# Kernel optimization log

Hardware: AMD Instinct MI355X
Metric: run time of the kernel (lower is better)

Reference implementation:

```python
import jax, jax.numpy as jnp
import numpy as np
from jax import lax

E_NUM, R_NUM = 100000, 500
ENT_DIM = 200
OUT_CH = 16
EPS = 1e-5


def _bn(x, s, b, m, v, axis):
    # eval-mode batchnorm; params broadcast along `axis`
    shape = [1] * x.ndim
    shape[axis] = x.shape[axis]
    s, b, m, v = (p.reshape(shape) for p in (s, b, m, v))
    return (x - m) * (s * lax.rsqrt(v + EPS)) + b


def setup_inputs() -> dict:
    key = jax.random.key(0)
    ks = jax.random.split(key, 12)
    B = 1024
    inp = {
        'entity_id': jax.random.randint(ks[0], (B,), 0, E_NUM),
        'relation_id': jax.random.randint(ks[1], (B,), 0, R_NUM),
        'ent_emb': jax.random.normal(ks[2], (E_NUM, ENT_DIM), jnp.float32) * 0.02,
        'rel_emb': jax.random.normal(ks[3], (R_NUM, ENT_DIM), jnp.float32) * 0.02,
        'filt_w': jax.random.normal(ks[4], (R_NUM, OUT_CH * 9), jnp.float32) * 0.1,
        'filt1_w': jax.random.normal(ks[5], (R_NUM, OUT_CH * 9), jnp.float32) * 0.1,
        'fc_w': jax.random.normal(ks[6], (ENT_DIM, 20 * 20 * OUT_CH * 2), jnp.float32) * 0.01,
        'fc_b': jnp.zeros((ENT_DIM,), jnp.float32),
        'out_bias': jnp.zeros((E_NUM,), jnp.float32),
    }
    for name, c, i in (('bn0', 1, 7), ('bn1', OUT_CH, 8), ('bn2', ENT_DIM, 9)):
        k1, k2, k3 = jax.random.split(ks[i], 3)
        inp[name + '_s'] = 1.0 + 0.1 * jax.random.normal(k1, (c,), jnp.float32)
        inp[name + '_b'] = 0.1 * jax.random.normal(k2, (c,), jnp.float32)
        inp[name + '_m'] = 0.1 * jax.random.normal(k3, (c,), jnp.float32)
        inp[name + '_v'] = jnp.ones((c,), jnp.float32)
    return inp


def reference(entity_id, relation_id, ent_emb, rel_emb, filt_w, filt1_w, fc_w, fc_b,
              out_bias, bn0_s, bn0_b, bn0_m, bn0_v, bn1_s, bn1_b, bn1_m, bn1_v,
              bn2_s, bn2_b, bn2_m, bn2_v):
    B = entity_id.shape[0]
    e = ent_emb[entity_id]                         # [B, 200]
    r = rel_emb[relation_id]                       # [B, 200]
    f = filt_w[relation_id].reshape(B * OUT_CH, 1, 3, 3)
    f1 = filt1_w[relation_id].reshape(B * OUT_CH, 1, 1, 9)

    x = jnp.concatenate([e, r], 1).reshape(B, 1, 10, 40)
    c0, c1, c2, c3 = jnp.split(x, 4, axis=3)       # each [B,1,10,10]
    t1 = jnp.swapaxes(c1, 2, 3)
    t2 = jnp.swapaxes(c3, 2, 3)
    m = jnp.concatenate([c0, c2], 2)               # [B,1,20,10]
    n = jnp.concatenate([t2, t1], 2)               # [B,1,20,10]
    x = jnp.concatenate([m, n], 3)                 # [B,1,20,20]

    x = _bn(x, bn0_s, bn0_b, bn0_m, bn0_v, axis=1)
    x = jnp.transpose(x, (1, 0, 2, 3))             # [1,B,20,20]

    dn = ('NCHW', 'OIHW', 'NCHW')
    x1 = lax.conv_general_dilated(x, f, (1, 1), [(1, 1), (1, 1)],
                                  dimension_numbers=dn, feature_group_count=B)
    x1 = _bn(x1.reshape(B, OUT_CH, 20, 20), bn1_s, bn1_b, bn1_m, bn1_v, axis=1)
    x2 = lax.conv_general_dilated(x, f1, (1, 1), [(0, 0), (4, 4)],
                                  dimension_numbers=dn, feature_group_count=B)
    x2 = _bn(x2.reshape(B, OUT_CH, 20, 20), bn1_s, bn1_b, bn1_m, bn1_v, axis=1)

    x = jax.nn.relu(jnp.concatenate([x1, x2], axis=1)).reshape(B, -1)  # [B,12800]
    x = x @ fc_w.T + fc_b                          # [B,200]
    x = _bn(x, bn2_s, bn2_b, bn2_m, bn2_v, axis=1)
    x = jax.nn.relu(x)
    logits = x @ ent_emb.T + out_bias              # [B, E_NUM]
    return jax.nn.sigmoid(logits)
```

## Files before the change

### kernel.cpp

```cpp
#include <hip/hip_runtime.h>
#include <hip/hip_bf16.h>

#define EPS 1e-5f

typedef __bf16 bf16x8 __attribute__((ext_vector_type(8)));
typedef float f32x4 __attribute__((ext_vector_type(4)));
typedef unsigned short ushort_t;

#define GLDS16(gp, lp) __builtin_amdgcn_global_load_lds( \
    (const __attribute__((address_space(1))) unsigned int*)(gp), \
    (__attribute__((address_space(3))) unsigned int*)(lp), 16, 0, 0)

__device__ __forceinline__ unsigned short f2bf(float f) {
    unsigned int u = __float_as_uint(f);
    u += 0x7fffu + ((u >> 16) & 1u);
    return (unsigned short)(u >> 16);
}

__device__ __forceinline__ void convert_pad_body(
    const float* __restrict__ src, ushort_t* __restrict__ dst,
    int R, int C, int R2, int C2, long long start, long long stride)
{
    int cpr = C2 >> 2;
    long long nchunks = (long long)R2 * cpr;
    for (long long idx = start; idx < nchunks; idx += stride) {
        int row = (int)(idx / cpr);
        int col = ((int)(idx - (long long)row * cpr)) << 2;
        float4 v = make_float4(0.f, 0.f, 0.f, 0.f);
        if (row < R && col < C)
            v = *reinterpret_cast<const float4*>(src + (size_t)row * C + col);
        union { unsigned short h[4]; uint2 u; } pk;
        pk.h[0] = f2bf(v.x); pk.h[1] = f2bf(v.y);
        pk.h[2] = f2bf(v.z); pk.h[3] = f2bf(v.w);
        *reinterpret_cast<uint2*>(dst + (size_t)row * C2 + col) = pk.u;
    }
}

__global__ __launch_bounds__(256) void prep_all_kernel(
    const float* __restrict__ fc_w, ushort_t* __restrict__ fcw,
    const int* __restrict__ eid, const int* __restrict__ rid,
    const float* __restrict__ ent_emb, const float* __restrict__ rel_emb,
    const float* __restrict__ filt_w, const float* __restrict__ filt1_w,
    const float* __restrict__ bn0_s, const float* __restrict__ bn0_b,
    const float* __restrict__ bn0_m, const float* __restrict__ bn0_v,
    const float* __restrict__ bn1_s, const float* __restrict__ bn1_b,
    const float* __restrict__ bn1_m, const float* __restrict__ bn1_v,
    ushort_t* __restrict__ act, ushort_t* __restrict__ E_bf)
{
    __shared__ float img[20][20];
    __shared__ float fA[16][9];
    __shared__ float fB[16][9];
    __shared__ float a1[16], b1[16];

    int t = threadIdx.x;
    if (blockIdx.x >= 4224) {
        long long start = (long long)(blockIdx.x - 4224) * 256 + t;
        convert_pad_body(ent_emb, E_bf, 100000, 200, 100000, 224, start, 21875LL * 256);
        return;
    }
    if (blockIdx.x >= 1024) {
        long long start = (long long)(blockIdx.x - 1024) * 256 + t;
        convert_pad_body(fc_w, fcw, 200, 12800, 256, 12800, start, 3200LL * 256);
        return;
    }

    int b = blockIdx.x;
    int e = eid[b], r = rid[b];

    float a0 = bn0_s[0] * rsqrtf(bn0_v[0] + EPS);
    float c0 = bn0_b[0] - bn0_m[0] * a0;

    for (int p = t; p < 400; p += 256) {
        int i = p / 20, j = p - (p / 20) * 20;
        int src;
        if (i < 10) src = (j < 10) ? (i * 40 + j) : ((j - 10) * 40 + 30 + i);
        else        src = (j < 10) ? ((i - 10) * 40 + 20 + j) : ((j - 10) * 40 + 10 + (i - 10));
        float v = (src < 200) ? ent_emb[(size_t)e * 200 + src]
                              : rel_emb[(size_t)r * 200 + (src - 200)];
        img[i][j] = v * a0 + c0;
    }
    for (int p = t; p < 144; p += 256) fA[p / 9][p % 9] = filt_w[(size_t)r * 144 + p];
    for (int p = t; p < 144; p += 256) fB[p / 9][p % 9] = filt1_w[(size_t)r * 144 + p];
    if (t < 16) {
        float a = bn1_s[t] * rsqrtf(bn1_v[t] + EPS);
        a1[t] = a;
        b1[t] = bn1_b[t] - bn1_m[t] * a;
    }
    __syncthreads();

    for (int idx = t; idx < 12800; idx += 256) {
        int c = idx / 400;
        int p = idx - c * 400;
        int i = p / 20, j = p - (p / 20) * 20;
        int ch = c & 15;
        float acc = 0.f;
        if (c < 16) {
            #pragma unroll
            for (int di = 0; di < 3; ++di) {
                int ii = i + di - 1;
                if (ii < 0 || ii >= 20) continue;
                #pragma unroll
                for (int dj = 0; dj < 3; ++dj) {
                    int jj = j + dj - 1;
                    if (jj >= 0 && jj < 20) acc += img[ii][jj] * fA[ch][di * 3 + dj];
                }
            }
        } else {
            #pragma unroll
            for (int dj = 0; dj < 9; ++dj) {
                int jj = j + dj - 4;
                if (jj >= 0 && jj < 20) acc += img[i][jj] * fB[ch][dj];
            }
        }
        float v = fmaxf(acc * a1[ch] + b1[ch], 0.f);
        act[(size_t)b * 12800 + idx] = f2bf(v);
    }
}

__global__ __launch_bounds__(256) void fc_gemm_kernel(
    const ushort_t* __restrict__ act,
    const ushort_t* __restrict__ fcw,
    float* __restrict__ part)
{
    __shared__ ushort_t lA[128 * 64];
    __shared__ ushort_t lB[64 * 64];

    int t = threadIdx.x;
    int bx = blockIdx.x;
    int mt = bx & 7;
    int nt = (bx >> 3) & 3;
    int ks = bx >> 5;
    int m0 = mt * 128, n0 = nt * 64, k0 = ks * 640;

    int lane = t & 63, w = t >> 6;
    int wm = (w >> 1) * 64;
    int wn = (w & 1) * 32;

    f32x4 acc[4][2] = {};

    for (int step = 0; step < 10; ++step) {
        int kk = k0 + step * 64;
        for (int c = w; c < 16; c += 4) {
            int elem = c * 512 + lane * 8;
            int row = elem >> 6, col = elem & 63;
            GLDS16(act + (size_t)(m0 + row) * 12800 + kk + col, lA + c * 512);
        }
        for (int c = w; c < 8; c += 4) {
            int elem = c * 512 + lane * 8;
            int row = elem >> 6, col = elem & 63;
            GLDS16(fcw + (size_t)(n0 + row) * 12800 + kk + col, lB + c * 512);
        }
        __syncthreads();
        #pragma unroll
        for (int kq = 0; kq < 2; ++kq) {
            bf16x8 af[4], bfr[2];
            #pragma unroll
            for (int mf = 0; mf < 4; ++mf) {
                int row = wm + mf * 16 + (lane & 15);
                af[mf] = *reinterpret_cast<const bf16x8*>(lA + row * 64 + kq * 32 + (lane >> 4) * 8);
            }
            #pragma unroll
            for (int nf = 0; nf < 2; ++nf) {
                int row = wn + nf * 16 + (lane & 15);
                bfr[nf] = *reinterpret_cast<const bf16x8*>(lB + row * 64 + kq * 32 + (lane >> 4) * 8);
            }
            #pragma unroll
            for (int mf = 0; mf < 4; ++mf)
                #pragma unroll
                for (int nf = 0; nf < 2; ++nf)
                    acc[mf][nf] = __builtin_amdgcn_mfma_f32_16x16x32_bf16(af[mf], bfr[nf], acc[mf][nf], 0, 0, 0);
        }
        __syncthreads();
    }

    float* outp = part + (size_t)ks * 1024 * 256;
    #pragma unroll
    for (int mf = 0; mf < 4; ++mf) {
        #pragma unroll
        for (int nf = 0; nf < 2; ++nf) {
            int colg = n0 + wn + nf * 16 + (lane & 15);
            int rowb = (lane >> 4) * 4;
            #pragma unroll
            for (int j = 0; j < 4; ++j) {
                int rowg = m0 + wm + mf * 16 + rowb + j;
                outp[(size_t)rowg * 256 + colg] = acc[mf][nf][j];
            }
        }
    }
}

__global__ __launch_bounds__(256) void reduce_bn2_kernel(
    const float* __restrict__ part, const float* __restrict__ fc_b,
    const float* __restrict__ bn2_s, const float* __restrict__ bn2_b,
    const float* __restrict__ bn2_m, const float* __restrict__ bn2_v,
    ushort_t* __restrict__ h)
{
    int idx = blockIdx.x * 256 + threadIdx.x;
    if (idx >= 1024 * 224) return;
    int m = idx / 224, n = idx - m * 224;
    float v = 0.f;
    if (n < 200) {
        float s = 0.f;
        #pragma unroll 4
        for (int k = 0; k < 20; ++k) s += part[(size_t)k * 1024 * 256 + (size_t)m * 256 + n];
        s += fc_b[n];
        float a = bn2_s[n] * rsqrtf(bn2_v[n] + EPS);
        v = fmaxf((s - bn2_m[n]) * a + bn2_b[n], 0.f);
    }
    h[idx] = f2bf(v);
}

__global__ __launch_bounds__(256) void big_gemm_kernel(
    const ushort_t* __restrict__ hm,
    const ushort_t* __restrict__ em,
    const float* __restrict__ out_bias,
    float* __restrict__ out)
{
    __shared__ ushort_t lA[2][128 * 32];
    __shared__ ushort_t lB[2][128 * 32];

    int phys = blockIdx.x;
    int virt = (phys & 7) * 782 + (phys >> 3);
    int mt = virt & 7;
    int nt = virt >> 3;
    int m0 = mt * 128, n0 = nt * 128;

    int t = threadIdx.x;
    int lane = t & 63, w = t >> 6;
    int wm = (w >> 1) * 64;
    int wn = (w & 1) * 64;

    f32x4 acc[4][4] = {};

    for (int c = w; c < 8; c += 4) {
        int row = c * 16 + (lane >> 2);
        int scol = ((lane & 3) ^ ((row >> 1) & 3)) * 8;
        GLDS16(hm + (size_t)(m0 + row) * 224 + scol, lA[0] + c * 512);
        int rowB = n0 + row; if (rowB > 99999) rowB = 99999;
        GLDS16(em + (size_t)rowB * 224 + scol, lB[0] + c * 512);
    }
    __syncthreads();

    for (int step = 0; step < 7; ++step) {
        int cur = step & 1;
        if (step < 6) {
            int kk = (step + 1) * 32;
            int nxt = cur ^ 1;
            for (int c = w; c < 8; c += 4) {
                int row = c * 16 + (lane >> 2);
                int scol = ((lane & 3) ^ ((row >> 1) & 3)) * 8;
                GLDS16(hm + (size_t)(m0 + row) * 224 + kk + scol, lA[nxt] + c * 512);
                int rowB = n0 + row; if (rowB > 99999) rowB = 99999;
                GLDS16(em + (size_t)rowB * 224 + kk + scol, lB[nxt] + c * 512);
            }
        }
        const ushort_t* A = lA[cur];
        const ushort_t* B = lB[cur];
        bf16x8 af[4], bfr[4];
        #pragma unroll
        for (int mf = 0; mf < 4; ++mf) {
            int r = wm + mf * 16 + (lane & 15);
            int pc = ((lane >> 4) ^ ((r >> 1) & 3)) * 8;
            af[mf] = *reinterpret_cast<const bf16x8*>(A + r * 32 + pc);
        }
        #pragma unroll
        for (int nf = 0; nf < 4; ++nf) {
            int r = wn + nf * 16 + (lane & 15);
            int pc = ((lane >> 4) ^ ((r >> 1) & 3)) * 8;
            bfr[nf] = *reinterpret_cast<const bf16x8*>(B + r * 32 + pc);
        }
        #pragma unroll
        for (int mf = 0; mf < 4; ++mf)
            #pragma unroll
            for (int nf = 0; nf < 4; ++nf)
                acc[mf][nf] = __builtin_amdgcn_mfma_f32_16x16x32_bf16(bfr[nf], af[mf], acc[mf][nf], 0, 0, 0);
        __syncthreads();
    }

    int ncol_base = n0 + wn + (lane >> 4) * 4;
    f32x4 b4[4];
    #pragma unroll
    for (int nf = 0; nf < 4; ++nf) {
        int colg = ncol_base + nf * 16;
        b4[nf] = (colg < 100000) ? *reinterpret_cast<const f32x4*>(out_bias + colg)
                                 : f32x4{0.f, 0.f, 0.f, 0.f};
    }
    #pragma unroll
    for (int mf = 0; mf < 4; ++mf) {
        int rowg = m0 + wm + mf * 16 + (lane & 15);
        float* orow = out + (size_t)rowg * 100000;
        #pragma unroll
        for (int nf = 0; nf < 4; ++nf) {
            int colg = ncol_base + nf * 16;
            if (colg < 100000) {
                f32x4 x = acc[mf][nf];
                f32x4 s;
                #pragma unroll
                for (int q = 0; q < 4; ++q)
                    s[q] = __builtin_amdgcn_rcpf(1.f + __expf(-(x[q] + b4[nf][q])));
                __builtin_nontemporal_store(s, reinterpret_cast<f32x4*>(orow + colg));
            }
        }
    }
}

extern "C" void kernel_launch(void* const* d_in, const int* in_sizes, int n_in,
                              void* d_out, int out_size, void* d_ws, size_t ws_size,
                              hipStream_t stream)
{
    const int*   eid      = (const int*)d_in[0];
    const int*   rid      = (const int*)d_in[1];
    const float* ent_emb  = (const float*)d_in[2];
    const float* rel_emb  = (const float*)d_in[3];
    const float* filt_w   = (const float*)d_in[4];
    const float* filt1_w  = (const float*)d_in[5];
    const float* fc_w     = (const float*)d_in[6];
    const float* fc_b     = (const float*)d_in[7];
    const float* out_bias = (const float*)d_in[8];
    const float* bn0_s = (const float*)d_in[9];
    const float* bn0_b = (const float*)d_in[10];
    const float* bn0_m = (const float*)d_in[11];
    const float* bn0_v = (const float*)d_in[12];
    const float* bn1_s = (const float*)d_in[13];
    const float* bn1_b = (const float*)d_in[14];
    const float* bn1_m = (const float*)d_in[15];
    const float* bn1_v = (const float*)d_in[16];
    const float* bn2_s = (const float*)d_in[17];
    const float* bn2_b = (const float*)d_in[18];
    const float* bn2_m = (const float*)d_in[19];
    const float* bn2_v = (const float*)d_in[20];
    float* out = (float*)d_out;

    char* ws = (char*)d_ws;
    ushort_t* E_bf = (ushort_t*)(ws + 0);
    ushort_t* act  = (ushort_t*)(ws + 44800000);
    ushort_t* fcw  = (ushort_t*)(ws + 71014400);
    float*    part = (float*)(ws + 77568000);
    ushort_t* hmat = (ushort_t*)(ws + 98539520);

    hipLaunchKernelGGL(prep_all_kernel, dim3(1024 + 3200 + 21875), dim3(256), 0, stream,
                       fc_w, fcw,
                       eid, rid, ent_emb, rel_emb, filt_w, filt1_w,
                       bn0_s, bn0_b, bn0_m, bn0_v, bn1_s, bn1_b, bn1_m, bn1_v, act, E_bf);
    hipLaunchKernelGGL(fc_gemm_kernel, dim3(640), dim3(256), 0, stream,
                       act, fcw, part);
    hipLaunchKernelGGL(reduce_bn2_kernel, dim3((1024 * 224) / 256), dim3(256), 0, stream,
                       part, fc_b, bn2_s, bn2_b, bn2_m, bn2_v, hmat);
    hipLaunchKernelGGL(big_gemm_kernel, dim3(782 * 8), dim3(256), 0, stream,
                       hmat, E_bf, out_bias, out);
}
```

Baseline: 209.5 us.

## Make big GEMM persistent and prefetch next tile's first K-slice

The output GEMM now launches 1280 persistent blocks that loop over the 6256 tiles with a grid stride, instead of one block per tile. During the last K step of each tile, the block prefetches the first K-slice of its next tile into the other LDS buffer, so that load overlaps the current MMA and epilogue. This removes per-block launch and prologue latency, at the cost of a possible tail imbalance (6256/1280 is not an integer) and less scheduler freedom across CUs.

```diff
diff --git a/kernel.cpp b/kernel.cpp
--- a/kernel.cpp
+++ b/kernel.cpp
@@ -219,88 +219,110 @@
     __shared__ ushort_t lA[2][128 * 32];
     __shared__ ushort_t lB[2][128 * 32];
 
-    int phys = blockIdx.x;
-    int virt = (phys & 7) * 782 + (phys >> 3);
-    int mt = virt & 7;
-    int nt = virt >> 3;
-    int m0 = mt * 128, n0 = nt * 128;
-
     int t = threadIdx.x;
     int lane = t & 63, w = t >> 6;
     int wm = (w >> 1) * 64;
     int wn = (w & 1) * 64;
-
-    f32x4 acc[4][4] = {};
-
-    for (int c = w; c < 8; c += 4) {
-        int row = c * 16 + (lane >> 2);
-        int scol = ((lane & 3) ^ ((row >> 1) & 3)) * 8;
-        GLDS16(hm + (size_t)(m0 + row) * 224 + scol, lA[0] + c * 512);
-        int rowB = n0 + row; if (rowB > 99999) rowB = 99999;
-        GLDS16(em + (size_t)rowB * 224 + scol, lB[0] + c * 512);
+    int srow = (lane >> 2);
+    int scol = ((lane & 3) ^ ((srow >> 1) & 3)) * 8;
+
+    int p = blockIdx.x;
+    int phase = 0;
+
+    {
+        int virt = (p & 7) * 782 + (p >> 3);
+        int m0 = (virt & 7) * 128, n0 = (virt >> 3) * 128;
+        for (int c = w; c < 8; c += 4) {
+            int row = c * 16 + srow;
+            GLDS16(hm + (size_t)(m0 + row) * 224 + scol, lA[0] + c * 512);
+            int rowB = n0 + row; if (rowB > 99999) rowB = 99999;
+            GLDS16(em + (size_t)rowB * 224 + scol, lB[0] + c * 512);
+        }
     }
     __syncthreads();
 
-    for (int step = 0; step < 7; ++step) {
-        int cur = step & 1;
-        if (step < 6) {
-            int kk = (step + 1) * 32;
+    for (int idx = p; idx < 6256; idx += 1280) {
+        int virt = (idx & 7) * 782 + (idx >> 3);
+        int m0 = (virt & 7) * 128, n0 = (virt >> 3) * 128;
+        int nidx = idx + 1280;
+        bool has_next = nidx < 6256;
+        int nm0 = 0, nn0 = 0;
+        if (has_next) {
+            int nvirt = (nidx & 7) * 782 + (nidx >> 3);
+            nm0 = (nvirt & 7) * 128; nn0 = (nvirt >> 3) * 128;
+        }
+
+        f32x4 acc[4][4] = {};
+
+        for (int step = 0; step < 7; ++step) {
+            int cur = (phase + step) & 1;
             int nxt = cur ^ 1;
-            for (int c = w; c < 8; c += 4) {
-                int row = c * 16 + (lane >> 2);
-                int scol = ((lane & 3) ^ ((row >> 1) & 3)) * 8;
-                GLDS16(hm + (size_t)(m0 + row) * 224 + kk + scol, lA[nxt] + c * 512);
-                int rowB = n0 + row; if (rowB > 99999) rowB = 99999;
-                GLDS16(em + (size_t)rowB * 224 + kk + scol, lB[nxt] + c * 512);
-            }
-        }
-        const ushort_t* A = lA[cur];
-        const ushort_t* B = lB[cur];
-        bf16x8 af[4], bfr[4];
-        #pragma unroll
-        for (int mf = 0; mf < 4; ++mf) {
-            int r = wm + mf * 16 + (lane & 15);
-            int pc = ((lane >> 4) ^ ((r >> 1) & 3)) * 8;
-            af[mf] = *reinterpret_cast<const bf16x8*>(A + r * 32 + pc);
-        }
-        #pragma unroll
-        for (int nf = 0; nf < 4; ++nf) {
-            int r = wn + nf * 16 + (lane & 15);
-            int pc = ((lane >> 4) ^ ((r >> 1) & 3)) * 8;
-            bfr[nf] = *reinterpret_cast<const bf16x8*>(B + r * 32 + pc);
-        }
-        #pragma unroll
-        for (int mf = 0; mf < 4; ++mf)
-            #pragma unroll
-            for (int nf = 0; nf < 4; ++nf)
-                acc[mf][nf] = __builtin_amdgcn_mfma_f32_16x16x32_bf16(bfr[nf], af[mf], acc[mf][nf], 0, 0, 0);
-        __syncthreads();
-    }
-
-    int ncol_base = n0 + wn + (lane >> 4) * 4;
-    f32x4 b4[4];
-    #pragma unroll
-    for (int nf = 0; nf < 4; ++nf) {
-        int colg = ncol_base + nf * 16;
-        b4[nf] = (colg < 100000) ? *reinterpret_cast<const f32x4*>(out_bias + colg)
-                                 : f32x4{0.f, 0.f, 0.f, 0.f};
-    }
-    #pragma unroll
-    for (int mf = 0; mf < 4; ++mf) {
-        int rowg = m0 + wm + mf * 16 + (lane & 15);
-        float* orow = out + (size_t)rowg * 100000;
+            if (step < 6) {
+                int kk = (step + 1) * 32;
+                for (int c = w; c < 8; c += 4) {
+                    int row = c * 16 + srow;
+                    GLDS16(hm + (size_t)(m0 + row) * 224 + kk + scol, lA[nxt] + c * 512);
+                    int rowB = n0 + row; if (rowB > 99999) rowB = 99999;
+                    GLDS16(em + (size_t)rowB * 224 + kk + scol, lB[nxt] + c * 512);
+                }
+            } else if (has_next) {
+                for (int c = w; c < 8; c += 4) {
+                    int row = c * 16 + srow;
+                    GLDS16(hm + (size_t)(nm0 + row) * 224 + scol, lA[nxt] + c * 512);
+                    int rowB = nn0 + row; if (rowB > 99999) rowB = 99999;
+                    GLDS16(em + (size_t)rowB * 224 + scol, lB[nxt] + c * 512);
+                }
+            }
+            const ushort_t* A = lA[cur];
+            const ushort_t* B = lB[cur];
+            bf16x8 af[4], bfr[4];
+            #pragma unroll
+            for (int mf = 0; mf < 4; ++mf) {
+                int r = wm + mf * 16 + (lane & 15);
+                int pc = ((lane >> 4) ^ ((r >> 1) & 3)) * 8;
+                af[mf] = *reinterpret_cast<const bf16x8*>(A + r * 32 + pc);
+            }
+            #pragma unroll
+            for (int nf = 0; nf < 4; ++nf) {
+                int r = wn + nf * 16 + (lane & 15);
+                int pc = ((lane >> 4) ^ ((r >> 1) & 3)) * 8;
+                bfr[nf] = *reinterpret_cast<const bf16x8*>(B + r * 32 + pc);
+            }
+            #pragma unroll
+            for (int mf = 0; mf < 4; ++mf)
+                #pragma unroll
+                for (int nf = 0; nf < 4; ++nf)
+                    acc[mf][nf] = __builtin_amdgcn_mfma_f32_16x16x32_bf16(bfr[nf], af[mf], acc[mf][nf], 0, 0, 0);
+            __syncthreads();
+        }
+
+        int ncol_base = n0 + wn + (lane >> 4) * 4;
+        f32x4 b4[4];
         #pragma unroll
         for (int nf = 0; nf < 4; ++nf) {
             int colg = ncol_base + nf * 16;
-            if (colg < 100000) {
-                f32x4 x = acc[mf][nf];
-                f32x4 s;
-                #pragma unroll
-                for (int q = 0; q < 4; ++q)
-                    s[q] = __builtin_amdgcn_rcpf(1.f + __expf(-(x[q] + b4[nf][q])));
-                __builtin_nontemporal_store(s, reinterpret_cast<f32x4*>(orow + colg));
-            }
-        }
+            b4[nf] = (colg < 100000) ? *reinterpret_cast<const f32x4*>(out_bias + colg)
+                                     : f32x4{0.f, 0.f, 0.f, 0.f};
+        }
+        #pragma unroll
+        for (int mf = 0; mf < 4; ++mf) {
+            int rowg = m0 + wm + mf * 16 + (lane & 15);
+            float* orow = out + (size_t)rowg * 100000;
+            #pragma unroll
+            for (int nf = 0; nf < 4; ++nf) {
+                int colg = ncol_base + nf * 16;
+                if (colg < 100000) {
+                    f32x4 x = acc[mf][nf];
+                    f32x4 s;
+                    #pragma unroll
+                    for (int q = 0; q < 4; ++q)
+                        s[q] = __builtin_amdgcn_rcpf(1.f + __expf(-(x[q] + b4[nf][q])));
+                    __builtin_nontemporal_store(s, reinterpret_cast<f32x4*>(orow + colg));
+                }
+            }
+        }
+
+        phase ^= 1;
     }
 }
 
@@ -346,6 +368,6 @@
                        act, fcw, part);
     hipLaunchKernelGGL(reduce_bn2_kernel, dim3((1024 * 224) / 256), dim3(256), 0, stream,
                        part, fc_b, bn2_s, bn2_b, bn2_m, bn2_v, hmat);
-    hipLaunchKernelGGL(big_gemm_kernel, dim3(782 * 8), dim3(256), 0, stream,
+    hipLaunchKernelGGL(big_gemm_kernel, dim3(1280), dim3(256), 0, stream,
                        hmat, E_bf, out_bias, out);
 }
```

After: 232.8 us. 11.1% more time.
